# Kernel optimization log

Measured on AMD Instinct MI355X. Metric: run time of the kernel, lower is better.

The kernel has to match this reference:

```python
import jax, jax.numpy as jnp
import numpy as np
from jax import lax

STEP = 0.1
N_TIMESTEPS = 50
BATCH = 500000


def _sir_eq(x, beta, gamma):
    # x: (B, 3) -> (B, 3). Faithful to SIR_eq_batch: returns state + increment.
    S, I, R = x[:, 0], x[:, 1], x[:, 2]
    n = x.sum(axis=1)
    inf = beta * S * I / n
    rec = gamma * I
    return jnp.stack((S - inf, I + inf - rec, R + rec), axis=1)


def setup_inputs() -> dict:
    key = jax.random.key(0)
    kx, = jax.random.split(key, 1)
    x = jax.random.uniform(kx, (BATCH, 3), dtype=jnp.float32) + 0.1  # positive populations
    beta = jnp.full((1,), 0.5, dtype=jnp.float32)
    gamma = jnp.full((1,), 0.5, dtype=jnp.float32)
    return {"x": x, "beta": beta, "gamma": gamma}


def reference(x, beta, gamma):
    b = beta[0]
    g = gamma[0]

    def step_fn(prev, _):
        k1 = _sir_eq(prev, b, g)
        k2 = _sir_eq(prev + STEP * k1 / 2, b, g)
        k3 = _sir_eq(prev + STEP * k2 / 2, b, g)
        k4 = _sir_eq(prev + STEP * k3, b, g)
        # NOTE: original code adds the RK combination to the initial x, not prev
        new = x + (STEP / 6) * (k1 + 2 * k2 + 2 * k3 + k4)
        return new, new

    _, rest = lax.scan(step_fn, x, None, length=N_TIMESTEPS - 1)  # (T-1, B, 3)
    traj = jnp.concatenate([x[None], rest], axis=0)  # (T, B, 3)
    return jnp.transpose(traj, (1, 0, 2))  # (B, T, 3)
```

## Files before the change

kernel.cpp:

```cpp
#include <hip/hip_runtime.h>


#define BATCH 500000
#define NT    50
#define NF    (NT * 3)
#define ROWS  64

struct F3 { float s, i, r; };

__device__ __forceinline__ F3 sir_eq(F3 v, float b, float g, float rn) {
    float inf = b * v.s * v.i * rn;
    float rec = g * v.i;
    F3 o;
    o.s = v.s - inf;
    o.i = v.i + inf - rec;
    o.r = v.r + rec;
    return o;
}

__device__ __forceinline__ F3 rk_step(F3 prev, F3 x0, float b, float g) {
    float n  = prev.s + prev.i + prev.r;
    float r1 = __builtin_amdgcn_rcpf(n);
    float r2 = r1 * 0.952380952f;
    float r3 = r1 * 0.950118765f;
    float r4 = r1 * 0.904772676f;

    F3 k1 = sir_eq(prev, b, g, r1);
    F3 a2 = { fmaf(0.05f, k1.s, prev.s), fmaf(0.05f, k1.i, prev.i), fmaf(0.05f, k1.r, prev.r) };
    F3 k2 = sir_eq(a2, b, g, r2);
    F3 a3 = { fmaf(0.05f, k2.s, prev.s), fmaf(0.05f, k2.i, prev.i), fmaf(0.05f, k2.r, prev.r) };
    F3 k3 = sir_eq(a3, b, g, r3);
    F3 a4 = { fmaf(0.10f, k3.s, prev.s), fmaf(0.10f, k3.i, prev.i), fmaf(0.10f, k3.r, prev.r) };
    F3 k4 = sir_eq(a4, b, g, r4);

    const float C = (float)(0.1 / 6.0);
    F3 nw;
    nw.s = fmaf(C, (k1.s + k4.s) + 2.0f * (k2.s + k3.s), x0.s);
    nw.i = fmaf(C, (k1.i + k4.i) + 2.0f * (k2.i + k3.i), x0.i);
    nw.r = fmaf(C, (k1.r + k4.r) + 2.0f * (k2.r + k3.r), x0.r);
    return nw;
}

__global__ __launch_bounds__(ROWS) void sir_rk4_kernel(
        const float* __restrict__ x,
        const float* __restrict__ beta,
        const float* __restrict__ gamma,
        float* __restrict__ out) {
    __shared__ __align__(16) float lds[ROWS * NF];

    const int lane  = threadIdx.x;
    const int row0  = blockIdx.x * ROWS;
    const int row   = row0 + lane;
    const int nrows = min(ROWS, BATCH - row0);
    const bool active = lane < nrows;

    const float b = beta[0];
    const float g = gamma[0];

    F3 xv = { 1.0f, 1.0f, 1.0f };
    if (active) {
        xv.s = x[(size_t)row * 3 + 0];
        xv.i = x[(size_t)row * 3 + 1];
        xv.r = x[(size_t)row * 3 + 2];
    }

    float* myrow = lds + lane * NF;
    myrow[0] = xv.s; myrow[1] = xv.i; myrow[2] = xv.r;

    F3 prev = xv;
    for (int s = 1; s < NT; ++s) {
        prev = rk_step(prev, xv, b, g);
        myrow[s * 3 + 0] = prev.s;
        myrow[s * 3 + 1] = prev.i;
        myrow[s * 3 + 2] = prev.r;
    }

    __syncthreads();

    const float4* l4 = (const float4*)lds;
    float4* o4 = reinterpret_cast<float4*>(out + (size_t)row0 * NF);
    const int total4 = nrows * NF / 4;
    for (int li = lane; li < total4; li += ROWS) {
        o4[li] = l4[li];
    }
}

extern "C" void kernel_launch(void* const* d_in, const int* in_sizes, int n_in,
                              void* d_out, int out_size, void* d_ws, size_t ws_size,
                              hipStream_t stream) {
    const float* x     = (const float*)d_in[0];
    const float* beta  = (const float*)d_in[1];
    const float* gamma = (const float*)d_in[2];
    float* out = (float*)d_out;

    const int grid = (BATCH + ROWS - 1) / ROWS;
    sir_rk4_kernel<<<grid, ROWS, 0, stream>>>(x, beta, gamma, out);
}
```

Before: 339.3 us.

## Split timestep staging into two LDS phases to halve shared memory

The trajectory is computed and staged in two chunks (26 then 24 timesteps), with each chunk flushed to global memory before the next is computed. This halves the per-block LDS footprint, so more blocks can be resident per CU and latency is better hidden. The cost is extra barriers, a switch from float4 to float2 stores, and per-element index division in the copy-out loops.

```diff
diff --git a/kernel.cpp b/kernel.cpp
--- a/kernel.cpp
+++ b/kernel.cpp
@@ -4,6 +4,8 @@
 #define BATCH 500000
 #define NT    50
 #define NF    (NT * 3)
+#define S0    26
+#define S1    24
 #define ROWS  64
 
 struct F3 { float s, i, r; };
@@ -46,7 +48,7 @@
         const float* __restrict__ beta,
         const float* __restrict__ gamma,
         float* __restrict__ out) {
-    __shared__ __align__(16) float lds[ROWS * NF];
+    __shared__ __align__(16) float lds[ROWS * S0 * 3];
 
     const int lane  = threadIdx.x;
     const int row0  = blockIdx.x * ROWS;
@@ -64,24 +66,58 @@
         xv.r = x[(size_t)row * 3 + 2];
     }
 
-    float* myrow = lds + lane * NF;
-    myrow[0] = xv.s; myrow[1] = xv.i; myrow[2] = xv.r;
-
+    {
+        float* myrow = lds + lane * (S0 * 3);
+        myrow[0] = xv.s; myrow[1] = xv.i; myrow[2] = xv.r;
+    }
     F3 prev = xv;
-    for (int s = 1; s < NT; ++s) {
+    for (int s = 1; s < S0; ++s) {
         prev = rk_step(prev, xv, b, g);
+        float* myrow = lds + lane * (S0 * 3);
         myrow[s * 3 + 0] = prev.s;
         myrow[s * 3 + 1] = prev.i;
         myrow[s * 3 + 2] = prev.r;
     }
-
     __syncthreads();
 
-    const float4* l4 = (const float4*)lds;
-    float4* o4 = reinterpret_cast<float4*>(out + (size_t)row0 * NF);
-    const int total4 = nrows * NF / 4;
-    for (int li = lane; li < total4; li += ROWS) {
-        o4[li] = l4[li];
+    {
+        const float2* l2 = (const float2*)lds;
+        const int per = S0 * 3 / 2;
+        const int total2 = nrows * per;
+        for (int it = 0; it < per; ++it) {
+            int li = it * ROWS + lane;
+            if (li < total2) {
+                int r  = li / per;
+                int gg = li - r * per;
+                *reinterpret_cast<float2*>(
+                    out + (size_t)(row0 + r) * NF + 2 * gg) = l2[li];
+            }
+        }
+    }
+    __syncthreads();
+
+    for (int s = 0; s < S1; ++s) {
+        prev = rk_step(prev, xv, b, g);
+        float* myrow = lds + lane * (S1 * 3);
+        myrow[s * 3 + 0] = prev.s;
+        myrow[s * 3 + 1] = prev.i;
+        myrow[s * 3 + 2] = prev.r;
+    }
+    __syncthreads();
+
+    {
+        const float2* l2 = (const float2*)lds;
+        const int per = S1 * 3 / 2;
+        const int total2 = nrows * per;
+        for (int it = 0; it < per; ++it) {
+            int li = it * ROWS + lane;
+            if (li < total2) {
+                int r  = li / per;
+                int gg = li - r * per;
+                *reinterpret_cast<float2*>(
+                    out + (size_t)(row0 + r) * NF + (S0 * 3) + 2 * gg) = l2[li];
+            }
+        }
     }
 }
 
```

Measured after the change: 392.0 us. +15.6%, slower.

## Replace LDS-staged output with direct per-thread float2 stores and larger blocks

Applied to the files above, without the earlier changes.

Removes the shared-memory trajectory buffer and barrier. Each thread now writes its trajectory straight to global memory in chunks of four timesteps using float2 stores. Block size grows from 64 to 256 threads. The aim is to lift the occupancy limit set by the large per-block LDS footprint, at the cost of strided, less coalesced global writes.

```diff
diff --git a/kernel.cpp b/kernel.cpp
--- a/kernel.cpp
+++ b/kernel.cpp
@@ -4,7 +4,7 @@
 #define BATCH 500000
 #define NT    50
 #define NF    (NT * 3)
-#define ROWS  64
+#define BLOCK 256
 
 struct F3 { float s, i, r; };
 
@@ -41,18 +41,13 @@
     return nw;
 }
 
-__global__ __launch_bounds__(ROWS) void sir_rk4_kernel(
+__global__ __launch_bounds__(BLOCK) void sir_rk4_kernel(
         const float* __restrict__ x,
         const float* __restrict__ beta,
         const float* __restrict__ gamma,
         float* __restrict__ out) {
-    __shared__ __align__(16) float lds[ROWS * NF];
-
-    const int lane  = threadIdx.x;
-    const int row0  = blockIdx.x * ROWS;
-    const int row   = row0 + lane;
-    const int nrows = min(ROWS, BATCH - row0);
-    const bool active = lane < nrows;
+    const int row = blockIdx.x * BLOCK + threadIdx.x;
+    const bool active = row < BATCH;
 
     const float b = beta[0];
     const float g = gamma[0];
@@ -64,24 +59,33 @@
         xv.r = x[(size_t)row * 3 + 2];
     }
 
-    float* myrow = lds + lane * NF;
-    myrow[0] = xv.s; myrow[1] = xv.i; myrow[2] = xv.r;
+    float* orow = out + (size_t)row * NF;
 
     F3 prev = xv;
-    for (int s = 1; s < NT; ++s) {
-        prev = rk_step(prev, xv, b, g);
-        myrow[s * 3 + 0] = prev.s;
-        myrow[s * 3 + 1] = prev.i;
-        myrow[s * 3 + 2] = prev.r;
-    }
-
-    __syncthreads();
-
-    const float4* l4 = (const float4*)lds;
-    float4* o4 = reinterpret_cast<float4*>(out + (size_t)row0 * NF);
-    const int total4 = nrows * NF / 4;
-    for (int li = lane; li < total4; li += ROWS) {
-        o4[li] = l4[li];
+    #pragma unroll
+    for (int gi = 0; gi < 13; ++gi) {
+        const int nsteps = (gi < 12) ? 4 : 2;
+        float buf[12];
+        #pragma unroll
+        for (int t = 0; t < 4; ++t) {
+            if (t >= nsteps) break;
+            if (gi == 0 && t == 0) {
+                buf[0] = xv.s; buf[1] = xv.i; buf[2] = xv.r;
+            } else {
+                prev = rk_step(prev, xv, b, g);
+                buf[t * 3 + 0] = prev.s;
+                buf[t * 3 + 1] = prev.i;
+                buf[t * 3 + 2] = prev.r;
+            }
+        }
+        if (active) {
+            #pragma unroll
+            for (int j = 0; j < 6; ++j) {
+                if (j >= nsteps * 3 / 2) break;
+                *reinterpret_cast<float2*>(orow + gi * 12 + 2 * j) =
+                    make_float2(buf[2 * j], buf[2 * j + 1]);
+            }
+        }
     }
 }
 
@@ -93,6 +97,6 @@
     const float* gamma = (const float*)d_in[2];
     float* out = (float*)d_out;
 
-    const int grid = (BATCH + ROWS - 1) / ROWS;
-    sir_rk4_kernel<<<grid, ROWS, 0, stream>>>(x, beta, gamma, out);
+    const int grid = (BATCH + BLOCK - 1) / BLOCK;
+    sir_rk4_kernel<<<grid, BLOCK, 0, stream>>>(x, beta, gamma, out);
 }
```

Result: slower. 411.2 us (+21.2%).

## Stream trajectory to global in time chunks to shrink LDS footprint

Applied to the files above, without the earlier changes.

Splits the 50 timesteps into chunks of 10, staging only one chunk per row in shared memory and flushing it to global with float2 stores after each chunk. This cuts per-block LDS from the full trajectory to a fifth, allowing many more resident waves per CU to hide latency. In exchange it adds barriers per chunk and narrower, less contiguous global stores.

```diff
diff --git a/kernel.cpp b/kernel.cpp
--- a/kernel.cpp
+++ b/kernel.cpp
@@ -4,6 +4,9 @@
 #define BATCH 500000
 #define NT    50
 #define NF    (NT * 3)
+#define TCH   10
+#define NCH   (NT / TCH)
+#define CF    (TCH * 3)
 #define ROWS  64
 
 struct F3 { float s, i, r; };
@@ -46,13 +49,14 @@
         const float* __restrict__ beta,
         const float* __restrict__ gamma,
         float* __restrict__ out) {
-    __shared__ __align__(16) float lds[ROWS * NF];
+    __shared__ __align__(16) float lds[ROWS * CF];
 
     const int lane  = threadIdx.x;
     const int row0  = blockIdx.x * ROWS;
     const int row   = row0 + lane;
     const int nrows = min(ROWS, BATCH - row0);
     const bool active = lane < nrows;
+    const bool fullblk = (nrows == ROWS);
 
     const float b = beta[0];
     const float g = gamma[0];
@@ -64,24 +68,48 @@
         xv.r = x[(size_t)row * 3 + 2];
     }
 
-    float* myrow = lds + lane * NF;
-    myrow[0] = xv.s; myrow[1] = xv.i; myrow[2] = xv.r;
+    float* myrow = lds + lane * CF;
+    F3 prev = xv;
 
-    F3 prev = xv;
-    for (int s = 1; s < NT; ++s) {
-        prev = rk_step(prev, xv, b, g);
-        myrow[s * 3 + 0] = prev.s;
-        myrow[s * 3 + 1] = prev.i;
-        myrow[s * 3 + 2] = prev.r;
-    }
+    for (int c = 0; c < NCH; ++c) {
+        if (c == 0) {
+            myrow[0] = xv.s; myrow[1] = xv.i; myrow[2] = xv.r;
+        } else {
+            prev = rk_step(prev, xv, b, g);
+            myrow[0] = prev.s; myrow[1] = prev.i; myrow[2] = prev.r;
+        }
+        #pragma unroll
+        for (int tt = 1; tt < TCH; ++tt) {
+            prev = rk_step(prev, xv, b, g);
+            myrow[tt * 3 + 0] = prev.s;
+            myrow[tt * 3 + 1] = prev.i;
+            myrow[tt * 3 + 2] = prev.r;
+        }
+        __syncthreads();
 
-    __syncthreads();
-
-    const float4* l4 = (const float4*)lds;
-    float4* o4 = reinterpret_cast<float4*>(out + (size_t)row0 * NF);
-    const int total4 = nrows * NF / 4;
-    for (int li = lane; li < total4; li += ROWS) {
-        o4[li] = l4[li];
+        const float2* l2 = (const float2*)lds;
+        if (fullblk) {
+            #pragma unroll
+            for (int it = 0; it < CF / 2; ++it) {
+                int li = it * ROWS + lane;
+                int r  = li / (CF / 2);
+                int gg = li - r * (CF / 2);
+                *reinterpret_cast<float2*>(
+                    out + (size_t)(row0 + r) * NF + c * CF + 2 * gg) = l2[li];
+            }
+        } else {
+            const int total2 = nrows * (CF / 2);
+            for (int it = 0; it < CF / 2; ++it) {
+                int li = it * ROWS + lane;
+                if (li < total2) {
+                    int r  = li / (CF / 2);
+                    int gg = li - r * (CF / 2);
+                    *reinterpret_cast<float2*>(
+                        out + (size_t)(row0 + r) * NF + c * CF + 2 * gg) = l2[li];
+                }
+            }
+        }
+        __syncthreads();
     }
 }
 
```

Measured after the change: 422.5 us. 1.25x slower.
